# Performance work log

Measured on AMD Instinct MI355X. Metric: run time of the kernel, lower is better.

Reference implementation:

```python
import jax, jax.numpy as jnp
import numpy as np
from math import factorial

N_NODES = 10000
N_EDGES = 320000
FEAT = 32
NBASIS = 8
RMAX = 6.0
ZMAX = 119


def _cg(j1, m1, j2, m2, j3, m3):
    if m1 + m2 != m3 or j3 < abs(j1 - j2) or j3 > j1 + j2:
        return 0.0
    f = lambda n: float(factorial(n))
    pre = ((2 * j3 + 1) * f(j1 + j2 - j3) * f(j1 - j2 + j3) * f(-j1 + j2 + j3) / f(j1 + j2 + j3 + 1)) ** 0.5
    pre *= (f(j3 + m3) * f(j3 - m3) * f(j1 - m1) * f(j1 + m1) * f(j2 - m2) * f(j2 + m2)) ** 0.5
    s = 0.0
    for k in range(j1 + j2 + j3 + 1):
        d = [k, j1 + j2 - j3 - k, j1 - m1 - k, j2 + m2 - k, j3 - j2 + m1 + k, j3 - j1 - m2 + k]
        if min(d) < 0:
            continue
        s += (-1) ** k / (f(d[0]) * f(d[1]) * f(d[2]) * f(d[3]) * f(d[4]) * f(d[5]))
    return pre * s


def _u_real(l):
    # complex->real spherical harmonics unitary transform
    U = np.zeros((2 * l + 1, 2 * l + 1), dtype=complex)
    s2 = 1.0 / np.sqrt(2.0)
    for m in range(-l, l + 1):
        i = m + l
        if m == 0:
            U[i, l] = 1.0
        elif m > 0:
            U[i, l + m] = ((-1) ** m) * s2
            U[i, l - m] = s2
        else:
            U[i, l + m] = 1j * s2
            U[i, l - m] = -1j * ((-1) ** m) * s2
    return U


def _real_cg():
    # real Clebsch-Gordan coupling coefficients for l<=2, shape (9,9,9), sparse
    off = [0, 1, 4]
    C = np.zeros((9, 9, 9))
    Us = [_u_real(l) for l in range(3)]
    for l1 in range(3):
        for l2 in range(3):
            for l3 in range(3):
                if l3 < abs(l1 - l2) or l3 > l1 + l2:
                    continue
                cg = np.zeros((2 * l1 + 1, 2 * l2 + 1, 2 * l3 + 1))
                for m1 in range(-l1, l1 + 1):
                    for m2 in range(-l2, l2 + 1):
                        m3 = m1 + m2
                        if abs(m3) <= l3:
                            cg[m1 + l1, m2 + l2, m3 + l3] = _cg(l1, m1, l2, m2, l3, m3)
                blk = np.einsum('ia,jb,kc,abc->ijk', Us[l1], Us[l2], np.conj(Us[l3]), cg.astype(complex))
                C[off[l1]:off[l1] + 2 * l1 + 1, off[l2]:off[l2] + 2 * l2 + 1, off[l3]:off[l3] + 2 * l3 + 1] = blk.real + blk.imag
    return C

CGC = jnp.asarray(_real_cg(), dtype=jnp.float32)
SL = [slice(0, 1), slice(1, 4), slice(4, 9)]
PATHS0 = [(0, 0, 0), (0, 1, 1), (0, 2, 2)]
PATHS1 = [(l1, l2, l3) for l1 in range(3) for l2 in range(3) for l3 in range(3) if abs(l1 - l2) <= l3 <= l1 + l2]
PATHS2 = [(0, 0, 0), (1, 1, 0), (2, 2, 0)]


def _real_sph(u):
    x, y, z = u[:, 0], u[:, 1], u[:, 2]
    c0 = 0.28209479177387814
    c1 = 0.4886025119029199
    c2a = 1.0925484305920792
    c2b = 0.31539156525252005
    c2c = 0.5462742152960396
    return jnp.stack([c0 * jnp.ones_like(x), c1 * y, c1 * z, c1 * x,
                      c2a * x * y, c2a * y * z, c2b * (3.0 * z * z - 1.0), c2a * x * z,
                      c2c * (x * x - y * y)], axis=-1)


def _message_pass(x, rad, Y, src, dst, W, paths, out_dim, n_nodes):
    # gather src node features -> per-edge CG tensor product with (radial x Ylm) basis -> scatter-add to dst
    xs = x[src, 0]  # (E, Dx, F)
    msg = jnp.zeros((rad.shape[0], out_dim, x.shape[-1]), x.dtype)
    for p, (l1, l2, l3) in enumerate(paths):
        w = rad @ W[p]  # (E, F) learned radial path weights
        contrib = jnp.einsum('abc,eaf,eb,ef->ecf', CGC[SL[l1], SL[l2], SL[l3]], xs[:, SL[l1], :], Y[:, SL[l2]], w)
        msg = msg.at[:, SL[l3], :].add(contrib)
    y = jax.ops.segment_sum(msg, dst, num_segments=n_nodes)
    return y[:, None]  # (N, 1, out_dim, F)


def _eadd(a, b):
    if a.shape[2] == b.shape[2]:
        return a + b
    if a.shape[2] < b.shape[2]:
        a, b = b, a
    return a.at[:, :, :b.shape[2], :].add(b)


def _edense(x, K, b):
    # equivariant Dense: shared kernel across degrees, bias only on scalar (l=0) channel
    y = jnp.einsum('npdf,fg->npdg', x, K)
    return y.at[:, :, 0, :].add(b)


def _esilu(x):
    # silu on scalars, sigmoid(scalar)-gated scaling on l>0 components (equivariant)
    if x.shape[2] == 1:
        return jax.nn.silu(x)
    s = x[:, :, 0:1, :]
    return jnp.concatenate([jax.nn.silu(s), x[:, :, 1:, :] * jax.nn.sigmoid(s)], axis=2)


def _forward(dr_vec, Z, neighbor_idxs, embed, wmp0, wmp1, wmp2, dk1, db1, dk2, db2):
    idx_i, idx_j = neighbor_idxs[0], neighbor_idxs[1]
    nN = Z.shape[0]
    r = jnp.sqrt(jnp.sum(dr_vec * dr_vec, axis=-1) + 1e-12)  # (E,)
    u = dr_vec / r[:, None]
    n = jnp.arange(1, NBASIS + 1, dtype=dr_vec.dtype)
    rad = jnp.sqrt(2.0 / RMAX) * jnp.sin(n * jnp.pi * r[:, None] / RMAX) / r[:, None]  # Bessel radial basis
    t = jnp.clip(r / RMAX, 0.0, 1.0 - 1e-6)
    cut = jnp.where(r < RMAX, jnp.exp(1.0 - 1.0 / (1.0 - t * t)), 0.0)  # smooth cutoff
    mask = (idx_i != idx_j).astype(dr_vec.dtype)  # mask padding/self edges
    rad = rad * (cut * mask)[:, None]
    Y = _real_sph(u)  # (E, 9)
    x = embed[Z][:, None, None, :]  # (N, 1, 1, F)
    for it, (paths, W) in enumerate([(PATHS0, wmp0), (PATHS1, wmp1), (PATHS2, wmp2)]):
        last = it == 2
        y = _message_pass(x, rad, Y, idx_j, idx_i, W, paths, 1 if last else 9, nN)
        if last:
            x = x[:, :, 0:1, :]  # change_max_degree_or_type -> scalars only
        y = _eadd(x, y)
        y = _edense(y, dk1[it], db1[it])
        y = _esilu(y)
        y = _edense(y, dk2[it], db2[it])
        x = _eadd(x, y)
    return x[:, 0, 0, :]


def setup_inputs():
    key = jax.random.key(0)
    ks = jax.random.split(key, 10)
    dr_vec = 2.0 * jax.random.normal(ks[0], (N_EDGES, 3), jnp.float32)
    Z = jax.random.randint(ks[1], (N_NODES,), 0, ZMAX)
    neighbor_idxs = jax.random.randint(ks[2], (2, N_EDGES), 0, N_NODES)
    embed = jax.random.normal(ks[3], (ZMAX, FEAT), jnp.float32)
    sB = 1.0 / np.sqrt(NBASIS)
    wmp0 = sB * jax.random.normal(ks[4], (len(PATHS0), NBASIS, FEAT), jnp.float32)
    wmp1 = sB * jax.random.normal(ks[5], (len(PATHS1), NBASIS, FEAT), jnp.float32)
    wmp2 = sB * jax.random.normal(ks[6], (len(PATHS2), NBASIS, FEAT), jnp.float32)
    sF = 1.0 / np.sqrt(FEAT)
    dense_k1 = sF * jax.random.normal(ks[7], (3, FEAT, FEAT), jnp.float32)
    dense_b1 = jnp.zeros((3, FEAT), jnp.float32)
    dense_k2 = 0.1 * sF * jax.random.normal(ks[8], (3, FEAT, FEAT), jnp.float32)
    dense_b2 = jnp.zeros((3, FEAT), jnp.float32)
    return {"dr_vec": dr_vec, "Z": Z, "neighbor_idxs": neighbor_idxs, "embed": embed,
            "wmp0": wmp0, "wmp1": wmp1, "wmp2": wmp2,
            "dense_k1": dense_k1, "dense_b1": dense_b1, "dense_k2": dense_k2, "dense_b2": dense_b2}


def reference(dr_vec, Z, neighbor_idxs, embed, wmp0, wmp1, wmp2, dense_k1, dense_b1, dense_k2, dense_b2):
    return _forward(dr_vec, Z, neighbor_idxs, embed, wmp0, wmp1, wmp2, dense_k1, dense_b1, dense_k2, dense_b2)
```

## Files before the change

kernel.cpp:

```cpp
#include <hip/hip_runtime.h>
#include <type_traits>
#include <cstdint>
#include <cstddef>

#define N_FEAT 32
#define NBASIS 8
#define SPAN   16
#define BSLOTS 8
#define BEDGES (SPAN*BSLOTS)

namespace cgc {

constexpr double dfact(int n){ double r=1.0; for(int i=2;i<=n;++i) r*=(double)i; return r; }

constexpr double dsqrt(double x){
  if(x<=0.0) return 0.0;
  double g = x>1.0 ? x : 1.0;
  for(int i=0;i<200;++i){ double ng = 0.5*(g + x/g); if(ng==g) break; g=ng; }
  return g;
}

constexpr double cg1(int j1,int m1,int j2,int m2,int j3,int m3){
  int adiff = j1-j2; if(adiff<0) adiff=-adiff;
  if(m1+m2!=m3 || j3<adiff || j3>j1+j2) return 0.0;
  double pre = dsqrt((double)(2*j3+1)*dfact(j1+j2-j3)*dfact(j1-j2+j3)*dfact(-j1+j2+j3)/dfact(j1+j2+j3+1));
  pre = pre*dsqrt(dfact(j3+m3)*dfact(j3-m3)*dfact(j1-m1)*dfact(j1+m1)*dfact(j2-m2)*dfact(j2+m2));
  double s=0.0;
  for(int k=0;k<=j1+j2+j3;++k){
    int d1=j1+j2-j3-k, d2=j1-m1-k, d3=j2+m2-k, d4=j3-j2+m1+k, d5=j3-j1-m2+k;
    if(d1<0||d2<0||d3<0||d4<0||d5<0) continue;
    double term = 1.0/(dfact(k)*dfact(d1)*dfact(d2)*dfact(d3)*dfact(d4)*dfact(d5));
    s += (k&1)? -term : term;
  }
  return pre*s;
}

struct Tab { float v[9][9][9]; };

constexpr Tab make(){
  Tab T{};
  int off[3]={0,1,4};
  double Ure[3][5][5]={}, Uim[3][5][5]={};
  const double s2 = dsqrt(0.5);
  for(int l=0;l<3;++l){
    for(int m=-l;m<=l;++m){
      int i=m+l;
      if(m==0){ Ure[l][i][l]=1.0; }
      else if(m>0){
        Ure[l][i][l+m] = ((m&1)? -1.0:1.0)*s2;
        Ure[l][i][l-m] = s2;
      } else {
        int am=-m;
        Uim[l][i][l+m] = s2;
        Uim[l][i][l-m] = -(((am&1)?-1.0:1.0))*s2;
      }
    }
  }
  for(int l1=0;l1<3;++l1) for(int l2=0;l2<3;++l2) for(int l3=0;l3<3;++l3){
    int lo = l1-l2; if(lo<0) lo=-lo;
    if(l3<lo || l3>l1+l2) continue;
    int d1=2*l1+1, d2=2*l2+1, d3=2*l3+1;
    double cg[5][5][5]={};
    for(int m1=-l1;m1<=l1;++m1) for(int m2=-l2;m2<=l2;++m2){
      int m3=m1+m2;
      if(m3>=-l3 && m3<=l3) cg[m1+l1][m2+l2][m3+l3] = cg1(l1,m1,l2,m2,l3,m3);
    }
    double t1re[5][5][5]={}, t1im[5][5][5]={};
    for(int a=0;a<d1;++a) for(int b=0;b<d2;++b) for(int k=0;k<d3;++k){
      double sre=0, sim=0;
      for(int c=0;c<d3;++c){
        double g=cg[a][b][c]; if(g==0.0) continue;
        sre += g*Ure[l3][k][c];
        sim -= g*Uim[l3][k][c];
      }
      t1re[a][b][k]=sre; t1im[a][b][k]=sim;
    }
    double t2re[5][5][5]={}, t2im[5][5][5]={};
    for(int a=0;a<d1;++a) for(int j=0;j<d2;++j) for(int k=0;k<d3;++k){
      double sre=0,sim=0;
      for(int b=0;b<d2;++b){
        double ur=Ure[l2][j][b], ui=Uim[l2][j][b];
        if(ur==0.0&&ui==0.0) continue;
        sre += ur*t1re[a][b][k]-ui*t1im[a][b][k];
        sim += ur*t1im[a][b][k]+ui*t1re[a][b][k];
      }
      t2re[a][j][k]=sre; t2im[a][j][k]=sim;
    }
    for(int i=0;i<d1;++i) for(int j=0;j<d2;++j) for(int k=0;k<d3;++k){
      double sre=0,sim=0;
      for(int a=0;a<d1;++a){
        double ur=Ure[l1][i][a], ui=Uim[l1][i][a];
        if(ur==0.0&&ui==0.0) continue;
        sre += ur*t2re[a][j][k]-ui*t2im[a][j][k];
        sim += ur*t2im[a][j][k]+ui*t2re[a][j][k];
      }
      T.v[off[l1]+i][off[l2]+j][off[l3]+k] = (float)(sre+sim);
    }
  }
  return T;
}

constexpr Tab T = make();

}

template<int I, int N, typename F>
__device__ __forceinline__ void sfor(F&& f){
  if constexpr (I < N){
    f(std::integral_constant<int,I>{});
    sfor<I+1,N>(static_cast<F&&>(f));
  }
}

constexpr int LOFF[3] = {0,1,4};

struct PS0 {
  static constexpr int NP=3;
  static constexpr int L[3][3]={{0,0,0},{0,1,1},{0,2,2}};
  static constexpr int ALO=0, AHI=1, OD=9, WOFF=0;
  static constexpr int MINW=4, DEPTH=8;
};
struct PS1a {
  static constexpr int NP=9;
  static constexpr int L[9][3]={{0,0,0},{0,1,1},{0,2,2},
                                {1,0,1},{1,1,0},{1,1,1},{1,1,2},{1,2,1},{1,2,2}};
  static constexpr int ALO=0, AHI=4, OD=9, WOFF=0;
  static constexpr int MINW=3, DEPTH=3;
};
struct PS1b {
  static constexpr int NP=6;
  static constexpr int L[6][3]={{2,0,2},{2,1,1},{2,1,2},{2,2,0},{2,2,1},{2,2,2}};
  static constexpr int ALO=4, AHI=9, OD=9, WOFF=9*NBASIS*N_FEAT;
  static constexpr int MINW=3, DEPTH=3;
};
struct PS2 {
  static constexpr int NP=3;
  static constexpr int L[3][3]={{0,0,0},{1,1,0},{2,2,0}};
  static constexpr int ALO=0, AHI=9, OD=1, WOFF=0;
  static constexpr int MINW=3, DEPTH=4;
};

__global__ void zero_kernel(int* __restrict__ a, int n){
  int i = blockIdx.x*256 + threadIdx.x;
  if(i<n) a[i]=0;
}

__global__ void count_kernel(const int* __restrict__ dst, int* __restrict__ cnt, int E){
  int e = blockIdx.x*256 + threadIdx.x;
  if(e<E) atomicAdd(&cnt[dst[e]], 1);
}

__global__ void __launch_bounds__(1024) scan_kernel(const int* __restrict__ cnt,
                                                    int* __restrict__ row_ptr,
                                                    int* __restrict__ cursor, int n){
  __shared__ int part[1024];
  const int tid = threadIdx.x;
  const int chunk = (n + 1023) >> 10;
  const int s0 = tid*chunk;
  const int s1 = (s0+chunk < n) ? s0+chunk : n;
  int s=0;
  for(int i=s0;i<s1;++i) s += cnt[i];
  part[tid]=s; __syncthreads();
  for(int off=1; off<1024; off<<=1){
    int v = 0;
    if(tid>=off) v = part[tid-off];
    __syncthreads();
    part[tid] += v;
    __syncthreads();
  }
  int run = part[tid] - s;
  for(int i=s0;i<s1;++i){
    int cv = cnt[i];
    row_ptr[i]=run; cursor[i]=run;
    run += cv;
  }
  if(tid==1023) row_ptr[n] = part[1023];
}

__global__ void fill_kernel(const int* __restrict__ dst, const int* __restrict__ src,
                            int* __restrict__ cursor, int* __restrict__ perm,
                            int* __restrict__ srcs, int* __restrict__ dsts, int E){
  int e = blockIdx.x*256 + threadIdx.x;
  if(e<E){
    int d = dst[e];
    int pos = atomicAdd(&cursor[d], 1);
    perm[e] = pos;
    srcs[pos] = src[e];
    dsts[pos] = d;
  }
}

__global__ void geom_kernel(const float* __restrict__ dr, const int* __restrict__ ii,
                            const int* __restrict__ jj, const int* __restrict__ perm,
                            float* __restrict__ radY, int E){
  int e = blockIdx.x*256 + threadIdx.x;
  if(e>=E) return;
  float dx=dr[3*e], dy=dr[3*e+1], dz=dr[3*e+2];
  float r2 = fmaf(dx,dx,fmaf(dy,dy,fmaf(dz,dz,1e-12f)));
  float r = sqrtf(r2);
  float inv = 1.f/r;
  float ux=dx*inv, uy=dy*inv, uz=dz*inv;
  float t = r*(1.f/6.f);
  t = fminf(fmaxf(t,0.f), 1.f-1e-6f);
  float cut = 0.f;
  if (r < 6.f) cut = expf(1.f - 1.f/(1.f - t*t));
  if (ii[e]==jj[e]) cut = 0.f;
  float base = 0.57735026918962576f * inv * cut;
  float* o = radY + (size_t)perm[e]*20;
  const float pir = 0.52359877559829887f * r;
  #pragma unroll
  for(int nb=1; nb<=8; ++nb) o[nb-1] = base * sinf((float)nb * pir);
  o[8]  = 0.28209479177387814f;
  o[9]  = 0.4886025119029199f*uy;
  o[10] = 0.4886025119029199f*uz;
  o[11] = 0.4886025119029199f*ux;
  o[12] = 1.0925484305920792f*ux*uy;
  o[13] = 1.0925484305920792f*uy*uz;
  o[14] = 0.31539156525252005f*(3.f*uz*uz-1.f);
  o[15] = 1.0925484305920792f*ux*uz;
  o[16] = 0.5462742152960396f*(ux*ux-uy*uy);
  o[17]=0.f; o[18]=0.f; o[19]=0.f;
}

__global__ void init_kernel(const float* __restrict__ embed, const int* __restrict__ Z,
                            float* __restrict__ xA, int nN){
  int i = blockIdx.x*256 + threadIdx.x;
  if(i >= nN*N_FEAT) return;
  int n = i>>5, f = i&31;
  xA[(size_t)n*288 + f] = embed[Z[n]*N_FEAT + f];
}

template<class PS>
__global__ void __launch_bounds__(256, PS::MINW) mp_kernel(
    const int* __restrict__ dsts, const int* __restrict__ srcs,
    const float* __restrict__ radY, const float* __restrict__ x_in,
    const float* __restrict__ W, float* __restrict__ ymsg, int E)
{
  constexpr int NP = PS::NP;
  constexpr int ALO = PS::ALO, AHI = PS::AHI, DA = AHI-ALO;
  constexpr int OD = PS::OD;
  constexpr int DEPTH = PS::DEPTH, NBUF = DEPTH+1;

  __shared__ float sRad[BEDGES*20];
  __shared__ int   sSrc[BEDGES];
  __shared__ int   sDst[BEDGES];

  const int tid  = threadIdx.x;
  const int base = blockIdx.x * BEDGES;
  const int nE   = (base + BEDGES <= E) ? BEDGES : (E - base);

  {
    const float4* g4 = (const float4*)(radY + (size_t)base*20);
    float4* s4 = (float4*)sRad;
    const int n4 = nE*5;
    for (int i=tid; i<n4; i+=256) s4[i] = g4[i];
    for (int i=tid; i<nE;  i+=256){ sSrc[i]=srcs[base+i]; sDst[i]=dsts[base+i]; }
  }
  __syncthreads();

  const int f  = tid & 31;
  const int k0 = (tid>>5)*SPAN;
  if (k0 >= nE) return;

  float Wreg[NP][NBASIS];
  sfor<0,NP>([&](auto P){
    sfor<0,NBASIS>([&](auto Q){
      Wreg[P.value][Q.value] = W[PS::WOFF + (P.value*NBASIS+Q.value)*N_FEAT + f];
    });
  });

  float msg[OD];
  sfor<0,OD>([&](auto C){ msg[C.value]=0.f; });

  auto gather = [&](float* dst, int k){
    const float* xb = x_in + (size_t)sSrc[k]*288 + ALO*N_FEAT + f;
    sfor<0,DA>([&](auto A){ dst[A.value] = xb[A.value*N_FEAT]; });
  };

  auto compute = [&](const float* xs, int k){
    const float* rp = sRad + k*20;
    const float4 q0 = *(const float4*)(rp);
    const float4 q1 = *(const float4*)(rp+4);
    const float4 q2 = *(const float4*)(rp+8);
    const float4 q3 = *(const float4*)(rp+12);
    const float y8 = rp[16];
    const float rad[8] = {q0.x,q0.y,q0.z,q0.w,q1.x,q1.y,q1.z,q1.w};
    const float Yv[9]  = {q2.x,q2.y,q2.z,q2.w,q3.x,q3.y,q3.z,q3.w,y8};
    sfor<0,NP>([&](auto P){
      constexpr int p  = P.value;
      constexpr int l1 = PS::L[p][0], l2 = PS::L[p][1], l3 = PS::L[p][2];
      constexpr int o1 = LOFF[l1], o2 = LOFF[l2], o3 = LOFF[l3];
      float w = 0.f;
      sfor<0,NBASIS>([&](auto Q){ w = fmaf(rad[Q.value], Wreg[p][Q.value], w); });
      sfor<0,2*l2+1>([&](auto B){
        constexpr int b = B.value;
        const float yw = Yv[o2+b]*w;
        sfor<0,2*l1+1>([&](auto A){
          constexpr int a = A.value;
          sfor<0,2*l3+1>([&](auto C){
            constexpr int c = C.value;
            constexpr float cgv = cgc::T.v[o1+a][o2+b][o3+c];
            if constexpr (cgv > 1e-7f || cgv < -1e-7f){
              msg[o3+c] = fmaf(cgv*xs[o1+a-ALO], yw, msg[o3+c]);
            }
          });
        });
      });
    });
  };

  auto flush = [&](int d){
    float* yb = ymsg + ((size_t)d*OD)*N_FEAT + f;
    sfor<0,OD>([&](auto C){
      atomicAdd(yb + C.value*N_FEAT, msg[C.value]);
      msg[C.value] = 0.f;
    });
  };

  if (nE == BEDGES){
    float buf[NBUF][DA];
    sfor<0,DEPTH>([&](auto J){ gather(buf[J.value], k0 + J.value); });
    int dcur = sDst[k0];
    sfor<0,SPAN>([&](auto I){
      constexpr int i = I.value;
      int dnext;
      if constexpr (i+1 < SPAN) dnext = sDst[k0+i+1]; else dnext = -1;
      if constexpr (i+DEPTH < SPAN) gather(buf[(i+DEPTH)%NBUF], k0+i+DEPTH);
      compute(buf[i%NBUF], k0+i);
      if (i == SPAN-1 || dnext != dcur) flush(dcur);
      dcur = dnext;
    });
  } else {
    const int k1 = (k0+SPAN < nE) ? k0+SPAN : nE;
    for (int k=k0; k<k1; ++k){
      float xs[DA];
      gather(xs, k);
      compute(xs, k);
      const int dc = sDst[k];
      const int dn = (k+1 < k1) ? sDst[k+1] : -1;
      if (dn != dc) flush(dc);
    }
  }
}

template<int DX>
__global__ void __launch_bounds__(256) nodeA_kernel(
    const float* __restrict__ xin, const float* __restrict__ ymsg,
    const float* __restrict__ K1, const float* __restrict__ b1,
    const float* __restrict__ K2, const float* __restrict__ b2,
    float* __restrict__ xout, int nN)
{
  __shared__ float sK1[1024], sK2[1024], sb1[32], sb2[32];
  __shared__ float tb[8][9][32];
  const int tid = threadIdx.x;
  for(int i=tid;i<1024;i+=256){ sK1[i]=K1[i]; sK2[i]=K2[i]; }
  if(tid<32){ sb1[tid]=b1[tid]; sb2[tid]=b2[tid]; }
  __syncthreads();
  const int h = tid>>5, f = tid&31;
  const int n = blockIdx.x*8 + h;
  const bool valid = n < nN;
  const int nc = valid ? n : 0;
  float xi[9];
  #pragma unroll
  for(int c=0;c<9;++c){
    float t = ymsg[((size_t)nc*9+c)*32+f];
    float x = 0.f;
    if (c<DX) x = xin[((size_t)nc*9+c)*32+f];
    xi[c]=x;
    tb[h][c][f] = t + x;
  }
  __syncthreads();
  float u[9];
  #pragma unroll
  for(int c=0;c<9;++c){
    float acc = (c==0) ? sb1[f] : 0.f;
    #pragma unroll
    for(int g=0;g<32;++g) acc = fmaf(tb[h][c][g], sK1[g*32+f], acc);
    u[c]=acc;
  }
  const float gate = 1.f/(1.f+expf(-u[0]));
  __syncthreads();
  #pragma unroll
  for(int c=0;c<9;++c) tb[h][c][f] = u[c]*gate;
  __syncthreads();
  #pragma unroll
  for(int c=0;c<9;++c){
    float acc = (c==0) ? sb2[f] : 0.f;
    #pragma unroll
    for(int g=0;g<32;++g) acc = fmaf(tb[h][c][g], sK2[g*32+f], acc);
    if (valid) xout[((size_t)n*9+c)*32+f] = acc + ((c<DX) ? xi[c] : 0.f);
  }
}

__global__ void __launch_bounds__(256) nodeB_kernel(
    const float* __restrict__ xin, const float* __restrict__ msg0,
    const float* __restrict__ K1, const float* __restrict__ b1,
    const float* __restrict__ K2, const float* __restrict__ b2,
    float* __restrict__ out, int nN)
{
  __shared__ float sK1[1024], sK2[1024], sb1[32], sb2[32];
  __shared__ float tb[8][32];
  const int tid = threadIdx.x;
  for(int i=tid;i<1024;i+=256){ sK1[i]=K1[i]; sK2[i]=K2[i]; }
  if(tid<32){ sb1[tid]=b1[tid]; sb2[tid]=b2[tid]; }
  __syncthreads();
  const int h = tid>>5, f = tid&31;
  const int n = blockIdx.x*8 + h;
  const bool valid = n < nN;
  const int nc = valid ? n : 0;
  const float x0 = xin[(size_t)nc*288 + f];
  tb[h][f] = msg0[(size_t)nc*32+f] + x0;
  __syncthreads();
  float acc = sb1[f];
  #pragma unroll
  for(int g=0;g<32;++g) acc = fmaf(tb[h][g], sK1[g*32+f], acc);
  const float gate = 1.f/(1.f+expf(-acc));
  const float v = acc*gate;
  __syncthreads();
  tb[h][f] = v;
  __syncthreads();
  float acc2 = sb2[f];
  #pragma unroll
  for(int g=0;g<32;++g) acc2 = fmaf(tb[h][g], sK2[g*32+f], acc2);
  if (valid) out[(size_t)n*32+f] = x0 + acc2;
}

extern "C" void kernel_launch(void* const* d_in, const int* in_sizes, int n_in,
                              void* d_out, int out_size, void* d_ws, size_t ws_size,
                              hipStream_t stream) {
  const float* dr    = (const float*)d_in[0];
  const int*   Z     = (const int*)  d_in[1];
  const int*   nbr   = (const int*)  d_in[2];
  const float* embed = (const float*)d_in[3];
  const float* wmp0  = (const float*)d_in[4];
  const float* wmp1  = (const float*)d_in[5];
  const float* wmp2  = (const float*)d_in[6];
  const float* dk1   = (const float*)d_in[7];
  const float* db1   = (const float*)d_in[8];
  const float* dk2   = (const float*)d_in[9];
  const float* db2   = (const float*)d_in[10];
  const int nN = in_sizes[1];
  const int E  = in_sizes[2]/2;
  const int* idx_i = nbr;
  const int* idx_j = nbr + E;

  uintptr_t base = (uintptr_t)d_ws;
  auto alloc = [&](size_t bytes)->void*{
    uintptr_t p = (base + 255) & ~(uintptr_t)255;
    base = p + bytes;
    return (void*)p;
  };
  float* radY    = (float*)alloc((size_t)E*20*4);
  int*   cnt     = (int*)  alloc((size_t)nN*4);
  int*   cursor  = (int*)  alloc((size_t)nN*4);
  int*   row_ptr = (int*)  alloc((size_t)(nN+1)*4);
  int*   perm    = (int*)  alloc((size_t)E*4);
  int*   srcs    = (int*)  alloc((size_t)E*4);
  int*   dsts    = (int*)  alloc((size_t)E*4);
  float* xA      = (float*)alloc((size_t)nN*288*4);
  float* xB      = (float*)alloc((size_t)nN*288*4);
  float* ymsg    = (float*)alloc((size_t)nN*288*4);

  const int gE = (E+255)/256;
  const int gN = (nN+255)/256;

  zero_kernel <<<gN, 256, 0, stream>>>(cnt, nN);
  count_kernel<<<gE, 256, 0, stream>>>(idx_i, cnt, E);
  scan_kernel <<<1, 1024, 0, stream>>>(cnt, row_ptr, cursor, nN);
  fill_kernel <<<gE, 256, 0, stream>>>(idx_i, idx_j, cursor, perm, srcs, dsts, E);

  geom_kernel <<<gE, 256, 0, stream>>>(dr, idx_i, idx_j, perm, radY, E);
  init_kernel <<<(nN*N_FEAT+255)/256, 256, 0, stream>>>(embed, Z, xA, nN);

  const int gND = (nN+7)/8;
  const int gMP = (E + BEDGES - 1) / BEDGES;
  const size_t ymsgBytes = (size_t)nN*288*4;

  hipMemsetAsync(ymsg, 0, ymsgBytes, stream);
  mp_kernel<PS0><<<gMP, 256, 0, stream>>>(dsts, srcs, radY, xA, wmp0, ymsg, E);
  nodeA_kernel<1><<<gND, 256, 0, stream>>>(xA, ymsg, dk1, db1, dk2, db2, xB, nN);
  hipMemsetAsync(ymsg, 0, ymsgBytes, stream);
  mp_kernel<PS1a><<<gMP, 256, 0, stream>>>(dsts, srcs, radY, xB, wmp1, ymsg, E);
  mp_kernel<PS1b><<<gMP, 256, 0, stream>>>(dsts, srcs, radY, xB, wmp1, ymsg, E);
  nodeA_kernel<9><<<gND, 256, 0, stream>>>(xB, ymsg, dk1+1024, db1+32, dk2+1024, db2+32, xA, nN);
  hipMemsetAsync(ymsg, 0, (size_t)nN*32*4, stream);
  mp_kernel<PS2><<<gMP, 256, 0, stream>>>(dsts, srcs, radY, xA, wmp2, ymsg, E);
  nodeB_kernel<<<gND, 256, 0, stream>>>(xA, ymsg, dk1+2048, db1+64, dk2+2048, db2+64,
                                        (float*)d_out, nN);
}
```

Baseline: 435.9 us.

## Merge layer-1 message-passing kernels and software-pipeline LDS edge loads

Fuses the two layer-1 message-passing launches (split over input l ranges) into a single kernel that handles all 15 paths. This removes the duplicated edge/radial reads and the second set of atomic flushes into the message buffer. The fused kernel uses a chunked, partly rolled loop with lower MINW to keep code size and register pressure manageable. Layers 0 and 2 gain a double-buffered prefetch of the next edge's radial/Y values and destination index from LDS, and layer 2 lowers its gather depth from 4 to 3. The cost is more registers per thread in the fused kernel, which may reduce occupancy.

```diff
diff --git a/kernel.cpp b/kernel.cpp
--- a/kernel.cpp
+++ b/kernel.cpp
@@ -119,25 +119,23 @@
   static constexpr int L[3][3]={{0,0,0},{0,1,1},{0,2,2}};
   static constexpr int ALO=0, AHI=1, OD=9, WOFF=0;
   static constexpr int MINW=4, DEPTH=8;
+  static constexpr bool LPRE=true;
 };
-struct PS1a {
-  static constexpr int NP=9;
-  static constexpr int L[9][3]={{0,0,0},{0,1,1},{0,2,2},
-                                {1,0,1},{1,1,0},{1,1,1},{1,1,2},{1,2,1},{1,2,2}};
-  static constexpr int ALO=0, AHI=4, OD=9, WOFF=0;
-  static constexpr int MINW=3, DEPTH=3;
-};
-struct PS1b {
-  static constexpr int NP=6;
-  static constexpr int L[6][3]={{2,0,2},{2,1,1},{2,1,2},{2,2,0},{2,2,1},{2,2,2}};
-  static constexpr int ALO=4, AHI=9, OD=9, WOFF=9*NBASIS*N_FEAT;
-  static constexpr int MINW=3, DEPTH=3;
+struct PS1 {
+  static constexpr int NP=15;
+  static constexpr int L[15][3]={{0,0,0},{0,1,1},{0,2,2},
+                                 {1,0,1},{1,1,0},{1,1,1},{1,1,2},{1,2,1},{1,2,2},
+                                 {2,0,2},{2,1,1},{2,1,2},{2,2,0},{2,2,1},{2,2,2}};
+  static constexpr int ALO=0, AHI=9, OD=9, WOFF=0;
+  static constexpr int MINW=2, DEPTH=3;
+  static constexpr bool LPRE=false;
 };
 struct PS2 {
   static constexpr int NP=3;
   static constexpr int L[3][3]={{0,0,0},{1,1,0},{2,2,0}};
   static constexpr int ALO=0, AHI=9, OD=1, WOFF=0;
-  static constexpr int MINW=3, DEPTH=4;
+  static constexpr int MINW=3, DEPTH=3;
+  static constexpr bool LPRE=true;
 };
 
 __global__ void zero_kernel(int* __restrict__ a, int n){
@@ -272,20 +270,25 @@
   float msg[OD];
   sfor<0,OD>([&](auto C){ msg[C.value]=0.f; });
 
-  auto gather = [&](float* dst, int k){
+  auto gather = [&](float (&dst)[DA], int k){
     const float* xb = x_in + (size_t)sSrc[k]*288 + ALO*N_FEAT + f;
     sfor<0,DA>([&](auto A){ dst[A.value] = xb[A.value*N_FEAT]; });
   };
 
-  auto compute = [&](const float* xs, int k){
+  auto ldsload = [&](float (&rr)[8], float (&yy)[9], int k){
     const float* rp = sRad + k*20;
     const float4 q0 = *(const float4*)(rp);
     const float4 q1 = *(const float4*)(rp+4);
     const float4 q2 = *(const float4*)(rp+8);
     const float4 q3 = *(const float4*)(rp+12);
-    const float y8 = rp[16];
-    const float rad[8] = {q0.x,q0.y,q0.z,q0.w,q1.x,q1.y,q1.z,q1.w};
-    const float Yv[9]  = {q2.x,q2.y,q2.z,q2.w,q3.x,q3.y,q3.z,q3.w,y8};
+    rr[0]=q0.x; rr[1]=q0.y; rr[2]=q0.z; rr[3]=q0.w;
+    rr[4]=q1.x; rr[5]=q1.y; rr[6]=q1.z; rr[7]=q1.w;
+    yy[0]=q2.x; yy[1]=q2.y; yy[2]=q2.z; yy[3]=q2.w;
+    yy[4]=q3.x; yy[5]=q3.y; yy[6]=q3.z; yy[7]=q3.w;
+    yy[8]=rp[16];
+  };
+
+  auto compute = [&](const float (&rad)[8], const float (&Yv)[9], const float (&xs)[DA]){
     sfor<0,NP>([&](auto P){
       constexpr int p  = P.value;
       constexpr int l1 = PS::L[p][0], l2 = PS::L[p][1], l3 = PS::L[p][2];
@@ -321,21 +324,59 @@
     float buf[NBUF][DA];
     sfor<0,DEPTH>([&](auto J){ gather(buf[J.value], k0 + J.value); });
     int dcur = sDst[k0];
-    sfor<0,SPAN>([&](auto I){
-      constexpr int i = I.value;
-      int dnext;
-      if constexpr (i+1 < SPAN) dnext = sDst[k0+i+1]; else dnext = -1;
-      if constexpr (i+DEPTH < SPAN) gather(buf[(i+DEPTH)%NBUF], k0+i+DEPTH);
-      compute(buf[i%NBUF], k0+i);
-      if (i == SPAN-1 || dnext != dcur) flush(dcur);
-      dcur = dnext;
-    });
+
+    if constexpr (PS::LPRE){
+      float pR[2][8], pY[2][9]; int pD[2];
+      ldsload(pR[0], pY[0], k0);
+      pD[0] = sDst[k0+1];
+      sfor<0,SPAN>([&](auto I){
+        constexpr int i = I.value;
+        if constexpr (i+1 < SPAN){
+          ldsload(pR[(i+1)%2], pY[(i+1)%2], k0+i+1);
+          if constexpr (i+2 < SPAN) pD[(i+1)%2] = sDst[k0+i+2];
+        }
+        if constexpr (i+DEPTH < SPAN) gather(buf[(i+DEPTH)%NBUF], k0+i+DEPTH);
+        compute(pR[i%2], pY[i%2], buf[i%NBUF]);
+        int dnext; if constexpr (i+1 < SPAN) dnext = pD[i%2]; else dnext = -1;
+        if (i == SPAN-1 || dnext != dcur) flush(dcur);
+        dcur = dnext;
+      });
+    } else {
+      static_assert(SPAN % 4 == 0 && NBUF == 4, "chunked path needs NBUF==4");
+      constexpr int NC = SPAN/4;
+      for (int c=0; c<NC-1; ++c){
+        const int kb = k0 + c*4;
+        sfor<0,4>([&](auto I){
+          constexpr int Iv = I.value;
+          const int k = kb + Iv;
+          gather(buf[(Iv+DEPTH)%NBUF], k+DEPTH);
+          float rr[8], yy[9];
+          ldsload(rr, yy, k);
+          compute(rr, yy, buf[Iv%NBUF]);
+          const int dnext = sDst[k+1];
+          if (dnext != dcur) flush(dcur);
+          dcur = dnext;
+        });
+      }
+      sfor<SPAN-4,SPAN>([&](auto I){
+        constexpr int i = I.value;
+        if constexpr (i+DEPTH < SPAN) gather(buf[(i+DEPTH)%NBUF], k0+i+DEPTH);
+        float rr[8], yy[9];
+        ldsload(rr, yy, k0+i);
+        compute(rr, yy, buf[i%NBUF]);
+        int dnext; if constexpr (i+1 < SPAN) dnext = sDst[k0+i+1]; else dnext = -1;
+        if (i == SPAN-1 || dnext != dcur) flush(dcur);
+        dcur = dnext;
+      });
+    }
   } else {
     const int k1 = (k0+SPAN < nE) ? k0+SPAN : nE;
     for (int k=k0; k<k1; ++k){
       float xs[DA];
       gather(xs, k);
-      compute(xs, k);
+      float rr[8], yy[9];
+      ldsload(rr, yy, k);
+      compute(rr, yy, xs);
       const int dc = sDst[k];
       const int dn = (k+1 < k1) ? sDst[k+1] : -1;
       if (dn != dc) flush(dc);
@@ -480,8 +521,7 @@
   mp_kernel<PS0><<<gMP, 256, 0, stream>>>(dsts, srcs, radY, xA, wmp0, ymsg, E);
   nodeA_kernel<1><<<gND, 256, 0, stream>>>(xA, ymsg, dk1, db1, dk2, db2, xB, nN);
   hipMemsetAsync(ymsg, 0, ymsgBytes, stream);
-  mp_kernel<PS1a><<<gMP, 256, 0, stream>>>(dsts, srcs, radY, xB, wmp1, ymsg, E);
-  mp_kernel<PS1b><<<gMP, 256, 0, stream>>>(dsts, srcs, radY, xB, wmp1, ymsg, E);
+  mp_kernel<PS1><<<gMP, 256, 0, stream>>>(dsts, srcs, radY, xB, wmp1, ymsg, E);
   nodeA_kernel<9><<<gND, 256, 0, stream>>>(xB, ymsg, dk1+1024, db1+32, dk2+1024, db2+32, xA, nN);
   hipMemsetAsync(ymsg, 0, (size_t)nN*32*4, stream);
   mp_kernel<PS2><<<gMP, 256, 0, stream>>>(dsts, srcs, radY, xA, wmp2, ymsg, E);
```

Measured after the change: 772.4 us. +77.2%, slower.

## Fuse CSR fill with geometry, pack src/dst indices, and merge zero with init

Applied to the files above, without the earlier changes.

The zero kernel is folded into the embedding init kernel, and the fill and geometry kernels are merged so each edge's sorted slot is taken by one atomic and radial/SH data is written there directly, which drops the perm array and row_ptr. Source and destination indices are packed into one int (16 bits each) to halve index traffic and shared memory in the message-passing kernels. The radial sines are computed with a Chebyshev recurrence from one fast sincos, and the cutoff uses the fast exp. PS2 pipeline depth drops from 4 to 3. The packing assumes node counts below 65536, and the fast intrinsics plus recurrence slightly change numerical accuracy.

```diff
diff --git a/kernel.cpp b/kernel.cpp
--- a/kernel.cpp
+++ b/kernel.cpp
@@ -137,12 +137,16 @@
   static constexpr int NP=3;
   static constexpr int L[3][3]={{0,0,0},{1,1,0},{2,2,0}};
   static constexpr int ALO=0, AHI=9, OD=1, WOFF=0;
-  static constexpr int MINW=3, DEPTH=4;
+  static constexpr int MINW=3, DEPTH=3;
 };
 
-__global__ void zero_kernel(int* __restrict__ a, int n){
+__global__ void init_kernel(const float* __restrict__ embed, const int* __restrict__ Z,
+                            float* __restrict__ xA, int* __restrict__ cnt, int nN){
   int i = blockIdx.x*256 + threadIdx.x;
-  if(i<n) a[i]=0;
+  if(i >= nN*N_FEAT) return;
+  int n = i>>5, f = i&31;
+  if(f==0) cnt[n]=0;
+  xA[(size_t)n*288 + f] = embed[Z[n]*N_FEAT + f];
 }
 
 __global__ void count_kernel(const int* __restrict__ dst, int* __restrict__ cnt, int E){
@@ -151,7 +155,6 @@
 }
 
 __global__ void __launch_bounds__(1024) scan_kernel(const int* __restrict__ cnt,
-                                                    int* __restrict__ row_ptr,
                                                     int* __restrict__ cursor, int n){
   __shared__ int part[1024];
   const int tid = threadIdx.x;
@@ -171,30 +174,20 @@
   int run = part[tid] - s;
   for(int i=s0;i<s1;++i){
     int cv = cnt[i];
-    row_ptr[i]=run; cursor[i]=run;
+    cursor[i]=run;
     run += cv;
   }
-  if(tid==1023) row_ptr[n] = part[1023];
-}
-
-__global__ void fill_kernel(const int* __restrict__ dst, const int* __restrict__ src,
-                            int* __restrict__ cursor, int* __restrict__ perm,
-                            int* __restrict__ srcs, int* __restrict__ dsts, int E){
-  int e = blockIdx.x*256 + threadIdx.x;
-  if(e<E){
-    int d = dst[e];
-    int pos = atomicAdd(&cursor[d], 1);
-    perm[e] = pos;
-    srcs[pos] = src[e];
-    dsts[pos] = d;
-  }
-}
-
-__global__ void geom_kernel(const float* __restrict__ dr, const int* __restrict__ ii,
-                            const int* __restrict__ jj, const int* __restrict__ perm,
-                            float* __restrict__ radY, int E){
+}
+
+__global__ void fillgeom_kernel(const int* __restrict__ dst, const int* __restrict__ src,
+                                const float* __restrict__ dr, int* __restrict__ cursor,
+                                int* __restrict__ srcsP, float* __restrict__ radY, int E){
   int e = blockIdx.x*256 + threadIdx.x;
   if(e>=E) return;
+  const int d = dst[e], s = src[e];
+  const int pos = atomicAdd(&cursor[d], 1);
+  srcsP[pos] = s | (d<<16);
+
   float dx=dr[3*e], dy=dr[3*e+1], dz=dr[3*e+2];
   float r2 = fmaf(dx,dx,fmaf(dy,dy,fmaf(dz,dz,1e-12f)));
   float r = sqrtf(r2);
@@ -203,13 +196,22 @@
   float t = r*(1.f/6.f);
   t = fminf(fmaxf(t,0.f), 1.f-1e-6f);
   float cut = 0.f;
-  if (r < 6.f) cut = expf(1.f - 1.f/(1.f - t*t));
-  if (ii[e]==jj[e]) cut = 0.f;
+  if (r < 6.f) cut = __expf(1.f - 1.f/(1.f - t*t));
+  if (d==s) cut = 0.f;
   float base = 0.57735026918962576f * inv * cut;
-  float* o = radY + (size_t)perm[e]*20;
+  float* o = radY + (size_t)pos*20;
   const float pir = 0.52359877559829887f * r;
-  #pragma unroll
-  for(int nb=1; nb<=8; ++nb) o[nb-1] = base * sinf((float)nb * pir);
+  float sT, cT;
+  __sincosf(pir, &sT, &cT);
+  const float twoc = 2.f*cT;
+  float sp = 0.f, sc = sT;
+  o[0] = base*sc;
+  #pragma unroll
+  for(int nb=2; nb<=8; ++nb){
+    float sn = fmaf(twoc, sc, -sp);
+    o[nb-1] = base*sn;
+    sp = sc; sc = sn;
+  }
   o[8]  = 0.28209479177387814f;
   o[9]  = 0.4886025119029199f*uy;
   o[10] = 0.4886025119029199f*uz;
@@ -222,31 +224,20 @@
   o[17]=0.f; o[18]=0.f; o[19]=0.f;
 }
 
-__global__ void init_kernel(const float* __restrict__ embed, const int* __restrict__ Z,
-                            float* __restrict__ xA, int nN){
-  int i = blockIdx.x*256 + threadIdx.x;
-  if(i >= nN*N_FEAT) return;
-  int n = i>>5, f = i&31;
-  xA[(size_t)n*288 + f] = embed[Z[n]*N_FEAT + f];
-}
-
 template<class PS>
-__global__ void __launch_bounds__(256, PS::MINW) mp_kernel(
-    const int* __restrict__ dsts, const int* __restrict__ srcs,
-    const float* __restrict__ radY, const float* __restrict__ x_in,
-    const float* __restrict__ W, float* __restrict__ ymsg, int E)
+__device__ __forceinline__ void mp_body(
+    int bid, float* sRad, int* sS,
+    const int* __restrict__ srcsP, const float* __restrict__ radY,
+    const float* __restrict__ x_in, const float* __restrict__ W,
+    float* __restrict__ ymsg, int E)
 {
   constexpr int NP = PS::NP;
   constexpr int ALO = PS::ALO, AHI = PS::AHI, DA = AHI-ALO;
   constexpr int OD = PS::OD;
   constexpr int DEPTH = PS::DEPTH, NBUF = DEPTH+1;
 
-  __shared__ float sRad[BEDGES*20];
-  __shared__ int   sSrc[BEDGES];
-  __shared__ int   sDst[BEDGES];
-
   const int tid  = threadIdx.x;
-  const int base = blockIdx.x * BEDGES;
+  const int base = bid * BEDGES;
   const int nE   = (base + BEDGES <= E) ? BEDGES : (E - base);
 
   {
@@ -254,7 +245,7 @@
     float4* s4 = (float4*)sRad;
     const int n4 = nE*5;
     for (int i=tid; i<n4; i+=256) s4[i] = g4[i];
-    for (int i=tid; i<nE;  i+=256){ sSrc[i]=srcs[base+i]; sDst[i]=dsts[base+i]; }
+    for (int i=tid; i<nE;  i+=256) sS[i] = srcsP[base+i];
   }
   __syncthreads();
 
@@ -272,12 +263,13 @@
   float msg[OD];
   sfor<0,OD>([&](auto C){ msg[C.value]=0.f; });
 
-  auto gather = [&](float* dst, int k){
-    const float* xb = x_in + (size_t)sSrc[k]*288 + ALO*N_FEAT + f;
+  auto gather = [&](float (&dst)[DA], int k){
+    const int s = sS[k] & 0xFFFF;
+    const float* xb = x_in + (size_t)s*288 + ALO*N_FEAT + f;
     sfor<0,DA>([&](auto A){ dst[A.value] = xb[A.value*N_FEAT]; });
   };
 
-  auto compute = [&](const float* xs, int k){
+  auto compute = [&](const float (&xs)[DA], int k){
     const float* rp = sRad + k*20;
     const float4 q0 = *(const float4*)(rp);
     const float4 q1 = *(const float4*)(rp+4);
@@ -320,15 +312,15 @@
   if (nE == BEDGES){
     float buf[NBUF][DA];
     sfor<0,DEPTH>([&](auto J){ gather(buf[J.value], k0 + J.value); });
-    int dcur = sDst[k0];
+    int vcur = sS[k0];
     sfor<0,SPAN>([&](auto I){
       constexpr int i = I.value;
-      int dnext;
-      if constexpr (i+1 < SPAN) dnext = sDst[k0+i+1]; else dnext = -1;
+      int vnext;
+      if constexpr (i+1 < SPAN) vnext = sS[k0+i+1]; else vnext = -1;
       if constexpr (i+DEPTH < SPAN) gather(buf[(i+DEPTH)%NBUF], k0+i+DEPTH);
       compute(buf[i%NBUF], k0+i);
-      if (i == SPAN-1 || dnext != dcur) flush(dcur);
-      dcur = dnext;
+      if (i == SPAN-1 || (vnext>>16) != (vcur>>16)) flush(vcur>>16);
+      vcur = vnext;
     });
   } else {
     const int k1 = (k0+SPAN < nE) ? k0+SPAN : nE;
@@ -336,11 +328,22 @@
       float xs[DA];
       gather(xs, k);
       compute(xs, k);
-      const int dc = sDst[k];
-      const int dn = (k+1 < k1) ? sDst[k+1] : -1;
+      const int dc = sS[k]>>16;
+      const int dn = (k+1 < k1) ? (sS[k+1]>>16) : -1;
       if (dn != dc) flush(dc);
     }
   }
+}
+
+template<class PS>
+__global__ void __launch_bounds__(256, PS::MINW) mp_kernel(
+    const int* __restrict__ srcsP, const float* __restrict__ radY,
+    const float* __restrict__ x_in, const float* __restrict__ W,
+    float* __restrict__ ymsg, int E)
+{
+  __shared__ float sRad[BEDGES*20];
+  __shared__ int   sS[BEDGES];
+  mp_body<PS>(blockIdx.x, sRad, sS, srcsP, radY, x_in, W, ymsg, E);
 }
 
 template<int DX>
@@ -453,38 +456,31 @@
   float* radY    = (float*)alloc((size_t)E*20*4);
   int*   cnt     = (int*)  alloc((size_t)nN*4);
   int*   cursor  = (int*)  alloc((size_t)nN*4);
-  int*   row_ptr = (int*)  alloc((size_t)(nN+1)*4);
-  int*   perm    = (int*)  alloc((size_t)E*4);
-  int*   srcs    = (int*)  alloc((size_t)E*4);
-  int*   dsts    = (int*)  alloc((size_t)E*4);
+  int*   srcsP   = (int*)  alloc((size_t)E*4);
   float* xA      = (float*)alloc((size_t)nN*288*4);
   float* xB      = (float*)alloc((size_t)nN*288*4);
   float* ymsg    = (float*)alloc((size_t)nN*288*4);
 
-  const int gE = (E+255)/256;
-  const int gN = (nN+255)/256;
-
-  zero_kernel <<<gN, 256, 0, stream>>>(cnt, nN);
-  count_kernel<<<gE, 256, 0, stream>>>(idx_i, cnt, E);
-  scan_kernel <<<1, 1024, 0, stream>>>(cnt, row_ptr, cursor, nN);
-  fill_kernel <<<gE, 256, 0, stream>>>(idx_i, idx_j, cursor, perm, srcs, dsts, E);
-
-  geom_kernel <<<gE, 256, 0, stream>>>(dr, idx_i, idx_j, perm, radY, E);
-  init_kernel <<<(nN*N_FEAT+255)/256, 256, 0, stream>>>(embed, Z, xA, nN);
-
+  const int gE  = (E+255)/256;
+  const int gI  = (nN*N_FEAT+255)/256;
   const int gND = (nN+7)/8;
   const int gMP = (E + BEDGES - 1) / BEDGES;
   const size_t ymsgBytes = (size_t)nN*288*4;
 
+  init_kernel    <<<gI, 256, 0, stream>>>(embed, Z, xA, cnt, nN);
+  count_kernel   <<<gE, 256, 0, stream>>>(idx_i, cnt, E);
+  scan_kernel    <<<1, 1024, 0, stream>>>(cnt, cursor, nN);
+  fillgeom_kernel<<<gE, 256, 0, stream>>>(idx_i, idx_j, dr, cursor, srcsP, radY, E);
+
   hipMemsetAsync(ymsg, 0, ymsgBytes, stream);
-  mp_kernel<PS0><<<gMP, 256, 0, stream>>>(dsts, srcs, radY, xA, wmp0, ymsg, E);
+  mp_kernel<PS0><<<gMP, 256, 0, stream>>>(srcsP, radY, xA, wmp0, ymsg, E);
   nodeA_kernel<1><<<gND, 256, 0, stream>>>(xA, ymsg, dk1, db1, dk2, db2, xB, nN);
   hipMemsetAsync(ymsg, 0, ymsgBytes, stream);
-  mp_kernel<PS1a><<<gMP, 256, 0, stream>>>(dsts, srcs, radY, xB, wmp1, ymsg, E);
-  mp_kernel<PS1b><<<gMP, 256, 0, stream>>>(dsts, srcs, radY, xB, wmp1, ymsg, E);
+  mp_kernel<PS1a><<<gMP, 256, 0, stream>>>(srcsP, radY, xB, wmp1, ymsg, E);
+  mp_kernel<PS1b><<<gMP, 256, 0, stream>>>(srcsP, radY, xB, wmp1, ymsg, E);
   nodeA_kernel<9><<<gND, 256, 0, stream>>>(xB, ymsg, dk1+1024, db1+32, dk2+1024, db2+32, xA, nN);
   hipMemsetAsync(ymsg, 0, (size_t)nN*32*4, stream);
-  mp_kernel<PS2><<<gMP, 256, 0, stream>>>(dsts, srcs, radY, xA, wmp2, ymsg, E);
+  mp_kernel<PS2><<<gMP, 256, 0, stream>>>(srcsP, radY, xA, wmp2, ymsg, E);
   nodeB_kernel<<<gND, 256, 0, stream>>>(xA, ymsg, dk1+2048, db1+64, dk2+2048, db2+64,
                                         (float*)d_out, nN);
 }
```

After: 426.7 us. -2.1%, faster.
